# Performance work log

Measured on AMD Instinct MI355X. Metric: run time of the kernel, lower is better.

The kernel has to match this reference:

```python
import jax, jax.numpy as jnp
import numpy as np

BATCH, L, N, D, SS, STEPS, GCN_OUT = 128, 24, 121, 121, 64, 6, 8
E = 1936

def _leaky(x):
    return jnp.where(x > 0, x, 0.01 * x)

def _layernorm(x, g, b, eps=1e-5):
    mu = jnp.mean(x, -1, keepdims=True)
    var = jnp.var(x, -1, keepdims=True)
    return (x - mu) * jax.lax.rsqrt(var + eps) * g + b

def setup_inputs() -> dict:
    key = jax.random.key(0)
    ks = jax.random.split(key, 20)
    nrm = lambda k, shape, s=0.05: jax.random.normal(k, shape, jnp.float32) * s
    z = lambda *s: jnp.zeros(s, jnp.float32)
    return {
        "x": jax.random.normal(ks[0], (BATCH, L, N), jnp.float32),
        "edge_index": jax.random.randint(ks[1], (2, E), 0, N, jnp.int32),
        "edge_attr": jax.random.uniform(ks[2], (E,), jnp.float32),
        # encoder ChebConv K=1 (= Linear(batch*l, 8)) + feature_compressor
        "conv_w": nrm(ks[3], (BATCH * L, GCN_OUT)), "conv_b": z(GCN_OUT),
        "comp_w1": nrm(ks[4], (2 * GCN_OUT, 32)), "comp_b1": z(32),
        "comp_w2": nrm(ks[5], (32, 1)), "comp_b2": z(1),
        # adapter Linear(121, d_model) + LayerNorm
        "adapter_w": nrm(ks[6], (N, D)), "adapter_b": z(D),
        "ln_g": jnp.ones((D,), jnp.float32), "ln_b": z(D),
        # mamba_insert params
        "lift_w1": nrm(ks[7], (D, 128)), "lift_b1": z(128),
        "lift_w2": nrm(ks[8], (128, D)), "lift_b2": z(D),
        "net_w1": nrm(ks[9], (2 * D, 128)), "net_b1": z(128),
        "net_w2": nrm(ks[10], (128, D)), "net_b2": z(D),
        "fc1_w": nrm(ks[11], (D, D)), "fc1_b": z(D),
        "fc2_w": nrm(ks[12], (D, SS)), "fc2_b": z(SS),
        "fc3_w": nrm(ks[13], (D, SS)), "fc3_b": z(SS),
        "A": nrm(ks[14], (D, SS), 0.3),
        "state_init": z(1, D, SS),
        "fcout_w": nrm(ks[15], (D, N)), "fcout_b": z(N),
    }

def reference(x, edge_index, edge_attr, conv_w, conv_b, comp_w1, comp_b1, comp_w2, comp_b2,
              adapter_w, adapter_b, ln_g, ln_b, lift_w1, lift_b1, lift_w2, lift_b2,
              net_w1, net_b1, net_w2, net_b2, fc1_w, fc1_b, fc2_w, fc2_b, fc3_w, fc3_b,
              A, state_init, fcout_w, fcout_b):
    b, l, n_nodes = x.shape
    # --- encoder: ChebConv(K=1) is a plain Linear; static and dynamic branches
    # use the identical input (x.view(-1,N).t()) and K=1 ignores edges, so they coincide.
    xg = x.reshape(-1, n_nodes).T                      # (N, b*l)
    g = xg @ conv_w + conv_b                           # (N, 8)
    comb = jnp.concatenate([g, g], axis=-1)            # (N, 16) static||dynamic
    feat = _leaky(comb @ comp_w1 + comp_b1) @ comp_w2 + comp_b2   # (N, 1)
    enc = jnp.broadcast_to(feat[:, 0][None, None, :], (b, l, n_nodes))  # repeat over (b,l)
    z0 = _layernorm(enc @ adapter_w + adapter_b, ln_g, ln_b)            # (b, l, D)

    def mamba(q, h_prev):
        lifted = jnp.tanh(jax.nn.relu(q @ lift_w1 + lift_b1) @ lift_w2 + lift_b2)
        xt = jax.nn.relu(jnp.concatenate([q, lifted], -1) @ net_w1 + net_b1) @ net_w2 + net_b2
        Bm = xt @ fc2_w + fc2_b                        # (b,l,n)
        Cm = xt @ fc3_w + fc3_b                        # (b,l,n)
        delta = jax.nn.softplus(xt @ fc1_w + fc1_b)    # (b,l,d)
        dA = jnp.exp(-jax.nn.celu(jnp.einsum('bld,dn->bldn', delta, A)))
        dB = delta[..., None] * Bm[:, :, None, :]      # (b,l,d,n)
        h_new = dA * h_prev[:, None] + xt[..., None] * dB
        out = jnp.einsum('bln,bldn->bld', Cm, h_new)
        return out, h_new[:, -1]

    h0 = jnp.broadcast_to(state_init, (b,) + state_init.shape[1:])
    _, h = mamba(z0, h0)                               # torch.no_grad warmup
    h = jax.lax.stop_gradient(h)
    q = z0
    outs = []
    for _ in range(STEPS):                             # steps <= 10 branch
        q, h = mamba(q, h)
        pred = q @ fcout_w + fcout_b                   # (b,l,m), m == D
        outs.append(pred)
        q = pred
    return jnp.stack(outs, axis=0)                     # (steps, b, l, m)
```

## Files before the change

### kernel.cpp

```cpp
#include <hip/hip_runtime.h>
#include <hip/hip_bf16.h>
#include <math.h>

#define BATCH 128
#define LSEQ 24
#define NN 121
#define SSZ 64
#define NSTEPS 6
#define BL 3072
#define NT 1024

typedef _Float16 h16;
typedef _Float16 h16x2 __attribute__((ext_vector_type(2)));
typedef float    fv8  __attribute__((ext_vector_type(8)));

#define OFF_WL1 0
#define OFF_WL2 16384
#define OFF_WN2 32768
#define OFF_WO  49152
#define OFF_WN1 65536
#define OFF_WF  98304
#define TOT_HALVES 131072

__device__ __forceinline__ h16x2 u2h(uint32_t u) {
    union { uint32_t u; h16x2 h; } c; c.u = u; return c.h;
}
__device__ __forceinline__ uint16_t f2u16(float v) {
    union { h16 h; uint16_t u; } c; c.h = (h16)v; return c.u;
}

__global__ __launch_bounds__(256) void enc_kernel(
    const float* __restrict__ x, const float* __restrict__ conv_w,
    const float* __restrict__ conv_b, const float* __restrict__ comp_w1,
    const float* __restrict__ comp_b1, const float* __restrict__ comp_w2,
    const float* __restrict__ comp_b2, float* __restrict__ feat_out)
{
    const int n = blockIdx.x;
    const int tid = threadIdx.x;
    float acc[8] = {0.f,0.f,0.f,0.f,0.f,0.f,0.f,0.f};
    for (int i = tid; i < BL; i += 256) {
        const float xv = x[i * NN + n];
        const float4* w4 = reinterpret_cast<const float4*>(conv_w + i * 8);
        const float4 a = w4[0], b = w4[1];
        acc[0] += xv * a.x; acc[1] += xv * a.y; acc[2] += xv * a.z; acc[3] += xv * a.w;
        acc[4] += xv * b.x; acc[5] += xv * b.y; acc[6] += xv * b.z; acc[7] += xv * b.w;
    }
    __shared__ float red[256][9];
    __shared__ float hred[32];
    #pragma unroll
    for (int j = 0; j < 8; ++j) red[tid][j] = acc[j];
    __syncthreads();
    for (int s = 128; s > 0; s >>= 1) {
        if (tid < s) {
            #pragma unroll
            for (int j = 0; j < 8; ++j) red[tid][j] += red[tid + s][j];
        }
        __syncthreads();
    }
    if (tid < 32) {
        float g[8];
        #pragma unroll
        for (int j = 0; j < 8; ++j) g[j] = red[0][j] + conv_b[j];
        float hsum = comp_b1[tid];
        #pragma unroll
        for (int j = 0; j < 8; ++j)
            hsum += g[j] * (comp_w1[j * 32 + tid] + comp_w1[(j + 8) * 32 + tid]);
        const float hv = hsum > 0.f ? hsum : 0.01f * hsum;
        hred[tid] = hv * comp_w2[tid];
    }
    __syncthreads();
    if (tid == 0) {
        float f = comp_b2[0];
        #pragma unroll
        for (int m = 0; m < 32; ++m) f += hred[m];
        feat_out[n] = f;
    }
}

__global__ __launch_bounds__(256) void prep_kernel(
    const float* __restrict__ lift_w1, const float* __restrict__ lift_w2,
    const float* __restrict__ net_w1,  const float* __restrict__ net_w2,
    const float* __restrict__ fc1_w,   const float* __restrict__ fc2_w,
    const float* __restrict__ fc3_w,   const float* __restrict__ fcout_w,
    uint16_t* __restrict__ ws16)
{
    const int i = blockIdx.x * 256 + threadIdx.x;
    if (i >= TOT_HALVES) return;
    float v = 0.f;
    if (i < OFF_WL2) {
        const int l = i, e = l & 1, j = (l >> 1) & 127, pp = l >> 8;
        const int rp = 2 * pp + e;
        if (rp < 121) v = lift_w1[rp * 128 + j];
    } else if (i < OFF_WN2) {
        const int l = i - OFF_WL2, e = l & 1, j = (l >> 1) & 127, pp = l >> 8;
        const int rp = 2 * pp + e;
        if (j < 121 && rp < 128) v = lift_w2[rp * 121 + j];
    } else if (i < OFF_WO) {
        const int l = i - OFF_WN2, e = l & 1, j = (l >> 1) & 127, pp = l >> 8;
        const int rp = 2 * pp + e;
        if (j < 121 && rp < 128) v = net_w2[rp * 121 + j];
    } else if (i < OFF_WN1) {
        const int l = i - OFF_WO, e = l & 1, j = (l >> 1) & 127, pp = l >> 8;
        const int rp = 2 * pp + e;
        if (j < 121 && rp < 121) v = fcout_w[rp * 121 + j];
    } else if (i < OFF_WF) {
        const int l = i - OFF_WN1, e = l & 1, j = (l >> 1) & 127, pp = l >> 8;
        const int rp = 2 * pp + e;
        const int o = rp < 121 ? rp : (rp >= 128 && rp < 249 ? rp - 7 : -1);
        if (o >= 0) v = net_w1[o * 128 + j];
    } else {
        const int l = i - OFF_WF, e = l & 1, j = (l >> 1) & 255, pp = l >> 9;
        const int rp = 2 * pp + e;
        if (rp < 121) {
            if (j < 121)                 v = fc1_w[rp * 121 + j];
            else if (j >= 128 && j < 192) v = fc2_w[rp * 64 + (j - 128)];
            else if (j >= 192)            v = fc3_w[rp * 64 + (j - 192)];
        }
    }
    ws16[i] = f2u16(v);
}

__device__ __forceinline__ float softplus_f(float v) {
    return v > 20.f ? v : log1pf(expf(v));
}

template<int ROWS, int COLS, int ACT>
__device__ __forceinline__ void matvec8(
    const float* __restrict__ W, const float* __restrict__ bias,
    const float* in, float* out, float* red, int tid)
{
    const int slice = tid >> 7;
    const int j = tid & 127;
    float a0 = 0.f;
    if (j < COLS) {
        const int r0 = (ROWS * slice) >> 3;
        const int r1 = (ROWS * (slice + 1)) >> 3;
        for (int i = r0; i < r1; ++i) a0 += in[i] * W[i * COLS + j];
    }
    red[tid] = a0;
    __syncthreads();
    if (tid < COLS) {
        float s = bias[tid];
        #pragma unroll
        for (int c = 0; c < 8; ++c) s += red[tid + 128 * c];
        if (ACT == 1) s = fmaxf(s, 0.f);
        else if (ACT == 2) s = tanhf(s);
        out[tid] = s;
    }
    __syncthreads();
}

template<int COLS, int ACT>
__device__ __forceinline__ void stream_mv(
    const uint32_t* __restrict__ g, const float* __restrict__ biasLds,
    const float* in, float* out, float* red, int tid)
{
    const int s = tid >> 7, j = tid & 127;
    float acc = 0.f;
    #pragma unroll
    for (int p = 0; p < 8; ++p) {
        const h16x2 h = u2h(g[(s * 8 + p) * 128 + j]);
        const int r = s * 16 + 2 * p;
        acc += in[r] * (float)h.x + in[r + 1] * (float)h.y;
    }
    red[tid] = acc;
    __syncthreads();
    if (tid < COLS) {
        float v = biasLds[tid];
        #pragma unroll
        for (int c = 0; c < 8; ++c) v += red[tid + 128 * c];
        if (ACT == 1) v = fmaxf(v, 0.f);
        else if (ACT == 2) v = tanhf(v);
        out[tid] = v;
    }
    __syncthreads();
}

__global__ __launch_bounds__(NT) void mamba_kernel(
    const float* __restrict__ adapter_w, const float* __restrict__ adapter_b,
    const float* __restrict__ ln_g, const float* __restrict__ ln_b,
    const float* __restrict__ lift_b1, const float* __restrict__ lift_b2,
    const float* __restrict__ net_b1,  const float* __restrict__ net_b2,
    const float* __restrict__ fc1_b,   const float* __restrict__ fc2_b,
    const float* __restrict__ fc3_b,   const float* __restrict__ fcout_b,
    const float* __restrict__ Aw, const float* __restrict__ state_init,
    const uint32_t* __restrict__ wsp,
    const float* __restrict__ feat_in, float* __restrict__ pred_out)
{
    __shared__ uint32_t WN1[16384];
    __shared__ uint32_t WF[16384];
    __shared__ __align__(16) float catP[256];
    __shared__ __align__(16) float t1[128], t2[128], xtsP[128], outvP[128];
    __shared__ float deltas[128], Bms[64], Cms[64];
    __shared__ float red[NT];
    __shared__ float r128[128], q128[128];
    __shared__ float lb1[128], lb2[128], nb1[128], nb2[128];
    __shared__ float f1b[128], f2b[64], f3b[64], fob[128];
    __shared__ float scal[2];

    const int tid = threadIdx.x;
    const uint32_t* WL1g = wsp;
    const uint32_t* WL2g = wsp + 8192;
    const uint32_t* WN2g = wsp + 16384;
    const uint32_t* WOg  = wsp + 24576;

    #pragma unroll
    for (int k = 0; k < 16; ++k) {
        WN1[k * NT + tid] = wsp[32768 + k * NT + tid];
        WF [k * NT + tid] = wsp[49152 + k * NT + tid];
    }

    const int hc = tid >> 7, hd = tid & 127;
    fv8 Areg, hreg;
    #pragma unroll
    for (int k = 0; k < 8; ++k) { Areg[k] = 0.f; hreg[k] = 0.f; }
    if (hd < NN) {
        #pragma unroll
        for (int k = 0; k < 8; ++k) {
            Areg[k] = Aw[hd * SSZ + hc * 8 + k];
            hreg[k] = state_init[hd * SSZ + hc * 8 + k];
        }
    }

    if (tid < 128) { lb1[tid] = lift_b1[tid]; nb1[tid] = net_b1[tid]; }
    if (tid < 121) {
        lb2[tid] = lift_b2[tid]; nb2[tid] = net_b2[tid];
        f1b[tid] = fc1_b[tid];   fob[tid] = fcout_b[tid];
        t1[tid] = feat_in[tid];
    }
    if (tid < 64) { f2b[tid] = fc2_b[tid]; f3b[tid] = fc3_b[tid]; }
    if (tid >= 121 && tid < 128) { catP[tid] = 0.f; xtsP[tid] = 0.f; outvP[tid] = 0.f; t2[tid] = 0.f; }
    if (tid >= 249 && tid < 256) catP[tid] = 0.f;
    __syncthreads();

    matvec8<NN, NN, 0>(adapter_w, adapter_b, t1, t2, red, tid);

    {
        if (tid < 128) {
            const float v = (tid < NN) ? t2[tid] : 0.f;
            r128[tid] = v; q128[tid] = v * v;
        }
        __syncthreads();
        for (int s = 64; s > 0; s >>= 1) {
            if (tid < s) { r128[tid] += r128[tid + s]; q128[tid] += q128[tid + s]; }
            __syncthreads();
        }
        if (tid == 0) {
            const float mu = r128[0] / (float)NN;
            const float var = q128[0] / (float)NN - mu * mu;
            scal[0] = mu; scal[1] = 1.0f / sqrtf(var + 1e-5f);
        }
        __syncthreads();
        if (tid < NN) catP[tid] = (t2[tid] - scal[0]) * scal[1] * ln_g[tid] + ln_b[tid];
        __syncthreads();
    }

    for (int ev = 0; ev < 7; ++ev) {
        stream_mv<128, 1>(WL1g, lb1, catP, t1, red, tid);
        stream_mv<121, 2>(WL2g, lb2, t1, catP + 128, red, tid);

        {
            const int s = tid >> 7, j = tid & 127;
            float acc = 0.f;
            #pragma unroll
            for (int p = 0; p < 16; ++p) {
                const h16x2 h = u2h(WN1[(s * 16 + p) * 128 + j]);
                const int r = s * 32 + 2 * p;
                acc += catP[r] * (float)h.x + catP[r + 1] * (float)h.y;
            }
            red[tid] = acc;
            __syncthreads();
            if (tid < 128) {
                float v = nb1[tid];
                #pragma unroll
                for (int c = 0; c < 8; ++c) v += red[tid + 128 * c];
                t2[tid] = fmaxf(v, 0.f);
            }
            __syncthreads();
        }

        stream_mv<121, 0>(WN2g, nb2, t2, xtsP, red, tid);

        {
            const int s = tid >> 8, j = tid & 255;
            float acc = 0.f;
            #pragma unroll
            for (int p = 0; p < 16; ++p) {
                const h16x2 h = u2h(WF[(s * 16 + p) * 256 + j]);
                const int r = s * 32 + 2 * p;
                acc += xtsP[r] * (float)h.x + xtsP[r + 1] * (float)h.y;
            }
            red[tid] = acc;
            __syncthreads();
            if (tid < 256) {
                const float val = red[tid] + red[tid + 256] + red[tid + 512] + red[tid + 768];
                if (tid < 121)
                    deltas[tid] = softplus_f(val + f1b[tid]);
                else if (tid >= 128 && tid < 192)
                    Bms[tid - 128] = val + f2b[tid - 128];
                else if (tid >= 192)
                    Cms[tid - 192] = val + f3b[tid - 192];
            }
            __syncthreads();
        }

        {
            float acc = 0.f;
            if (hd < NN) {
                const float dd = deltas[hd];
                const float coef = xtsP[hd] * dd;
                #pragma unroll
                for (int k = 0; k < 8; ++k) {
                    const float s = dd * Areg[k];
                    const float cel = s > 0.f ? s : expm1f(s);
                    const float dAv = expf(-cel);
                    const float hn = dAv * hreg[k] + coef * Bms[hc * 8 + k];
                    hreg[k] = hn;
                    acc += Cms[hc * 8 + k] * hn;
                }
            }
            red[tid] = acc;
            __syncthreads();
            if (tid < NN) {
                float s = 0.f;
                #pragma unroll
                for (int c = 0; c < 8; ++c) s += red[tid + 128 * c];
                outvP[tid] = s;
            }
            __syncthreads();
        }

        if (ev > 0) {
            stream_mv<121, 0>(WOg, fob, outvP, catP, red, tid);
            if (tid < NN) pred_out[(ev - 1) * NN + tid] = catP[tid];
            __syncthreads();
        }
    }
}

__global__ __launch_bounds__(256) void bcast_kernel(
    const float* __restrict__ pred, float* __restrict__ out)
{
    __shared__ float p[128];
    const int blk = blockIdx.x;
    const int s = blk / 24, chunk = blk - s * 24;
    const int t = threadIdx.x;
    if (t < NN) p[t] = pred[s * NN + t];
    __syncthreads();
    float* dst = out + ((long)s * BL + (long)chunk * 128) * NN;
    for (int idx = t; idx < 128 * NN; idx += 256)
        dst[idx] = p[idx % NN];
}

extern "C" void kernel_launch(void* const* d_in, const int* in_sizes, int n_in,
                              void* d_out, int out_size, void* d_ws, size_t ws_size,
                              hipStream_t stream)
{
    const float* x        = (const float*)d_in[0];
    const float* conv_w   = (const float*)d_in[3];
    const float* conv_b   = (const float*)d_in[4];
    const float* comp_w1  = (const float*)d_in[5];
    const float* comp_b1  = (const float*)d_in[6];
    const float* comp_w2  = (const float*)d_in[7];
    const float* comp_b2  = (const float*)d_in[8];
    const float* adapter_w= (const float*)d_in[9];
    const float* adapter_b= (const float*)d_in[10];
    const float* ln_g     = (const float*)d_in[11];
    const float* ln_b     = (const float*)d_in[12];
    const float* lift_w1  = (const float*)d_in[13];
    const float* lift_b1  = (const float*)d_in[14];
    const float* lift_w2  = (const float*)d_in[15];
    const float* lift_b2  = (const float*)d_in[16];
    const float* net_w1   = (const float*)d_in[17];
    const float* net_b1   = (const float*)d_in[18];
    const float* net_w2   = (const float*)d_in[19];
    const float* net_b2   = (const float*)d_in[20];
    const float* fc1_w    = (const float*)d_in[21];
    const float* fc1_b    = (const float*)d_in[22];
    const float* fc2_w    = (const float*)d_in[23];
    const float* fc2_b    = (const float*)d_in[24];
    const float* fc3_w    = (const float*)d_in[25];
    const float* fc3_b    = (const float*)d_in[26];
    const float* Aw       = (const float*)d_in[27];
    const float* state_in = (const float*)d_in[28];
    const float* fcout_w  = (const float*)d_in[29];
    const float* fcout_b  = (const float*)d_in[30];

    float* ws   = (float*)d_ws;
    float* feat = ws;
    float* pred = ws + 128;
    uint16_t* w16 = (uint16_t*)((char*)d_ws + 4096);
    const uint32_t* w32 = (const uint32_t*)w16;

    enc_kernel<<<NN, 256, 0, stream>>>(x, conv_w, conv_b, comp_w1, comp_b1,
                                       comp_w2, comp_b2, feat);
    prep_kernel<<<TOT_HALVES / 256, 256, 0, stream>>>(
        lift_w1, lift_w2, net_w1, net_w2, fc1_w, fc2_w, fc3_w, fcout_w, w16);
    mamba_kernel<<<1, NT, 0, stream>>>(adapter_w, adapter_b, ln_g, ln_b,
        lift_b1, lift_b2, net_b1, net_b2, fc1_b, fc2_b, fc3_b, fcout_b,
        Aw, state_in, w32, feat, pred);
    bcast_kernel<<<NSTEPS * 24, 256, 0, stream>>>(pred, (float*)d_out);
}
```

Baseline: 174.9 us.

## Drop weight-prep kernel; pack LDS weights in-kernel and stream fp32 weights directly

Removes the separate prep kernel that converted and repacked weights to fp16 in a workspace. The mamba kernel now builds the packed fp16 LDS copies of net_w1 and fc1/fc2/fc3 itself from the raw fp32 inputs. The per-step streamed matvecs read fp32 weights straight from global memory with bounds predicates. This removes one kernel launch and a global round-trip, but doubles the bytes streamed per step in the single-block serial loop and adds strided gathers at kernel start.

```diff
diff --git a/kernel.cpp b/kernel.cpp
--- a/kernel.cpp
+++ b/kernel.cpp
@@ -14,19 +14,12 @@
 typedef _Float16 h16x2 __attribute__((ext_vector_type(2)));
 typedef float    fv8  __attribute__((ext_vector_type(8)));
 
-#define OFF_WL1 0
-#define OFF_WL2 16384
-#define OFF_WN2 32768
-#define OFF_WO  49152
-#define OFF_WN1 65536
-#define OFF_WF  98304
-#define TOT_HALVES 131072
-
 __device__ __forceinline__ h16x2 u2h(uint32_t u) {
     union { uint32_t u; h16x2 h; } c; c.u = u; return c.h;
 }
-__device__ __forceinline__ uint16_t f2u16(float v) {
-    union { h16 h; uint16_t u; } c; c.h = (h16)v; return c.u;
+__device__ __forceinline__ uint32_t pack2(float a, float b) {
+    union { h16 h; uint16_t u; } x, y; x.h = (h16)a; y.h = (h16)b;
+    return (uint32_t)x.u | ((uint32_t)y.u << 16);
 }
 
 __global__ __launch_bounds__(256) void enc_kernel(
@@ -77,49 +70,6 @@
     }
 }
 
-__global__ __launch_bounds__(256) void prep_kernel(
-    const float* __restrict__ lift_w1, const float* __restrict__ lift_w2,
-    const float* __restrict__ net_w1,  const float* __restrict__ net_w2,
-    const float* __restrict__ fc1_w,   const float* __restrict__ fc2_w,
-    const float* __restrict__ fc3_w,   const float* __restrict__ fcout_w,
-    uint16_t* __restrict__ ws16)
-{
-    const int i = blockIdx.x * 256 + threadIdx.x;
-    if (i >= TOT_HALVES) return;
-    float v = 0.f;
-    if (i < OFF_WL2) {
-        const int l = i, e = l & 1, j = (l >> 1) & 127, pp = l >> 8;
-        const int rp = 2 * pp + e;
-        if (rp < 121) v = lift_w1[rp * 128 + j];
-    } else if (i < OFF_WN2) {
-        const int l = i - OFF_WL2, e = l & 1, j = (l >> 1) & 127, pp = l >> 8;
-        const int rp = 2 * pp + e;
-        if (j < 121 && rp < 128) v = lift_w2[rp * 121 + j];
-    } else if (i < OFF_WO) {
-        const int l = i - OFF_WN2, e = l & 1, j = (l >> 1) & 127, pp = l >> 8;
-        const int rp = 2 * pp + e;
-        if (j < 121 && rp < 128) v = net_w2[rp * 121 + j];
-    } else if (i < OFF_WN1) {
-        const int l = i - OFF_WO, e = l & 1, j = (l >> 1) & 127, pp = l >> 8;
-        const int rp = 2 * pp + e;
-        if (j < 121 && rp < 121) v = fcout_w[rp * 121 + j];
-    } else if (i < OFF_WF) {
-        const int l = i - OFF_WN1, e = l & 1, j = (l >> 1) & 127, pp = l >> 8;
-        const int rp = 2 * pp + e;
-        const int o = rp < 121 ? rp : (rp >= 128 && rp < 249 ? rp - 7 : -1);
-        if (o >= 0) v = net_w1[o * 128 + j];
-    } else {
-        const int l = i - OFF_WF, e = l & 1, j = (l >> 1) & 255, pp = l >> 9;
-        const int rp = 2 * pp + e;
-        if (rp < 121) {
-            if (j < 121)                 v = fc1_w[rp * 121 + j];
-            else if (j >= 128 && j < 192) v = fc2_w[rp * 64 + (j - 128)];
-            else if (j >= 192)            v = fc3_w[rp * 64 + (j - 192)];
-        }
-    }
-    ws16[i] = f2u16(v);
-}
-
 __device__ __forceinline__ float softplus_f(float v) {
     return v > 20.f ? v : log1pf(expf(v));
 }
@@ -150,18 +100,19 @@
     __syncthreads();
 }
 
-template<int COLS, int ACT>
-__device__ __forceinline__ void stream_mv(
-    const uint32_t* __restrict__ g, const float* __restrict__ biasLds,
+template<int R, int COLS, int ACT>
+__device__ __forceinline__ void stream_mv32(
+    const float* __restrict__ W, const float* __restrict__ biasLds,
     const float* in, float* out, float* red, int tid)
 {
     const int s = tid >> 7, j = tid & 127;
+    const bool jv = (j < COLS);
     float acc = 0.f;
     #pragma unroll
-    for (int p = 0; p < 8; ++p) {
-        const h16x2 h = u2h(g[(s * 8 + p) * 128 + j]);
-        const int r = s * 16 + 2 * p;
-        acc += in[r] * (float)h.x + in[r + 1] * (float)h.y;
+    for (int q = 0; q < 16; ++q) {
+        const int r = s * 16 + q;
+        const bool v = jv && (r < R);
+        acc += v ? in[r] * W[r * COLS + j] : 0.f;
     }
     red[tid] = acc;
     __syncthreads();
@@ -179,12 +130,15 @@
 __global__ __launch_bounds__(NT) void mamba_kernel(
     const float* __restrict__ adapter_w, const float* __restrict__ adapter_b,
     const float* __restrict__ ln_g, const float* __restrict__ ln_b,
-    const float* __restrict__ lift_b1, const float* __restrict__ lift_b2,
-    const float* __restrict__ net_b1,  const float* __restrict__ net_b2,
-    const float* __restrict__ fc1_b,   const float* __restrict__ fc2_b,
-    const float* __restrict__ fc3_b,   const float* __restrict__ fcout_b,
+    const float* __restrict__ lift_w1, const float* __restrict__ lift_b1,
+    const float* __restrict__ lift_w2, const float* __restrict__ lift_b2,
+    const float* __restrict__ net_w1,  const float* __restrict__ net_b1,
+    const float* __restrict__ net_w2,  const float* __restrict__ net_b2,
+    const float* __restrict__ fc1_w,   const float* __restrict__ fc1_b,
+    const float* __restrict__ fc2_w,   const float* __restrict__ fc2_b,
+    const float* __restrict__ fc3_w,   const float* __restrict__ fc3_b,
+    const float* __restrict__ fcout_w, const float* __restrict__ fcout_b,
     const float* __restrict__ Aw, const float* __restrict__ state_init,
-    const uint32_t* __restrict__ wsp,
     const float* __restrict__ feat_in, float* __restrict__ pred_out)
 {
     __shared__ uint32_t WN1[16384];
@@ -199,15 +153,35 @@
     __shared__ float scal[2];
 
     const int tid = threadIdx.x;
-    const uint32_t* WL1g = wsp;
-    const uint32_t* WL2g = wsp + 8192;
-    const uint32_t* WN2g = wsp + 16384;
-    const uint32_t* WOg  = wsp + 24576;
 
     #pragma unroll
     for (int k = 0; k < 16; ++k) {
-        WN1[k * NT + tid] = wsp[32768 + k * NT + tid];
-        WF [k * NT + tid] = wsp[49152 + k * NT + tid];
+        const int i = k * NT + tid;
+        const int pg = i >> 7, j = i & 127;
+        const int rp0 = 2 * pg, rp1 = rp0 + 1;
+        const int o0 = rp0 < 121 ? rp0 : (rp0 >= 128 && rp0 < 249 ? rp0 - 7 : -1);
+        const int o1 = rp1 < 121 ? rp1 : (rp1 >= 128 && rp1 < 249 ? rp1 - 7 : -1);
+        const float v0 = (o0 >= 0) ? net_w1[o0 * 128 + j] : 0.f;
+        const float v1 = (o1 >= 0) ? net_w1[o1 * 128 + j] : 0.f;
+        WN1[i] = pack2(v0, v1);
+    }
+    #pragma unroll
+    for (int k = 0; k < 16; ++k) {
+        const int i = k * NT + tid;
+        const int pg = i >> 8, j = i & 255;
+        const int rp0 = 2 * pg, rp1 = rp0 + 1;
+        float v0 = 0.f, v1 = 0.f;
+        if (j < 121) {
+            if (rp0 < 121) v0 = fc1_w[rp0 * 121 + j];
+            if (rp1 < 121) v1 = fc1_w[rp1 * 121 + j];
+        } else if (j >= 128 && j < 192) {
+            if (rp0 < 121) v0 = fc2_w[rp0 * 64 + (j - 128)];
+            if (rp1 < 121) v1 = fc2_w[rp1 * 64 + (j - 128)];
+        } else if (j >= 192) {
+            if (rp0 < 121) v0 = fc3_w[rp0 * 64 + (j - 192)];
+            if (rp1 < 121) v1 = fc3_w[rp1 * 64 + (j - 192)];
+        }
+        WF[i] = pack2(v0, v1);
     }
 
     const int hc = tid >> 7, hd = tid & 127;
@@ -256,8 +230,8 @@
     }
 
     for (int ev = 0; ev < 7; ++ev) {
-        stream_mv<128, 1>(WL1g, lb1, catP, t1, red, tid);
-        stream_mv<121, 2>(WL2g, lb2, t1, catP + 128, red, tid);
+        stream_mv32<121, 128, 1>(lift_w1, lb1, catP, t1, red, tid);
+        stream_mv32<128, 121, 2>(lift_w2, lb2, t1, catP + 128, red, tid);
 
         {
             const int s = tid >> 7, j = tid & 127;
@@ -279,7 +253,7 @@
             __syncthreads();
         }
 
-        stream_mv<121, 0>(WN2g, nb2, t2, xtsP, red, tid);
+        stream_mv32<128, 121, 0>(net_w2, nb2, t2, xtsP, red, tid);
 
         {
             const int s = tid >> 8, j = tid & 255;
@@ -331,7 +305,7 @@
         }
 
         if (ev > 0) {
-            stream_mv<121, 0>(WOg, fob, outvP, catP, red, tid);
+            stream_mv32<121, 121, 0>(fcout_w, fob, outvP, catP, red, tid);
             if (tid < NN) pred_out[(ev - 1) * NN + tid] = catP[tid];
             __syncthreads();
         }
@@ -389,15 +363,12 @@
     float* ws   = (float*)d_ws;
     float* feat = ws;
     float* pred = ws + 128;
-    uint16_t* w16 = (uint16_t*)((char*)d_ws + 4096);
-    const uint32_t* w32 = (const uint32_t*)w16;
 
     enc_kernel<<<NN, 256, 0, stream>>>(x, conv_w, conv_b, comp_w1, comp_b1,
                                        comp_w2, comp_b2, feat);
-    prep_kernel<<<TOT_HALVES / 256, 256, 0, stream>>>(
-        lift_w1, lift_w2, net_w1, net_w2, fc1_w, fc2_w, fc3_w, fcout_w, w16);
     mamba_kernel<<<1, NT, 0, stream>>>(adapter_w, adapter_b, ln_g, ln_b,
-        lift_b1, lift_b2, net_b1, net_b2, fc1_b, fc2_b, fc3_b, fcout_b,
-        Aw, state_in, w32, feat, pred);
+        lift_w1, lift_b1, lift_w2, lift_b2, net_w1, net_b1, net_w2, net_b2,
+        fc1_w, fc1_b, fc2_w, fc2_b, fc3_w, fc3_b, fcout_w, fcout_b,
+        Aw, state_in, feat, pred);
     bcast_kernel<<<NSTEPS * 24, 256, 0, stream>>>(pred, (float*)d_out);
 }
```

Result: slower. 282.5 us (+61.6%).
